# Optimization experiments

Measured on AMD Instinct MI355X. Metric: run time of the kernel, lower is better.

The kernel has to match this reference:

```python
import jax, jax.numpy as jnp
import numpy as np

B, S, HID, H = 4, 1024, 1024, 16
D = HID // H


def setup_inputs() -> dict:
    key = jax.random.key(0)
    ks = jax.random.split(key, 4)
    scale = 0.02
    return {
        "hidden_states": jax.random.normal(ks[0], (B, S, HID), dtype=jnp.float32),
        "attention_mask": jnp.ones((B, S), dtype=jnp.int32),
        "layer_head_mask": jnp.ones((H,), dtype=jnp.float32),
        "Wq": jax.random.normal(ks[1], (HID, HID), dtype=jnp.float32) * scale,
        "bq": jnp.zeros((HID,), dtype=jnp.float32),
        "Wk": jax.random.normal(ks[2], (HID, HID), dtype=jnp.float32) * scale,
        "bk": jnp.zeros((HID,), dtype=jnp.float32),
        "Wv": jax.random.normal(ks[3], (HID, HID), dtype=jnp.float32) * scale,
        "bv": jnp.zeros((HID,), dtype=jnp.float32),
    }


def reference(hidden_states, attention_mask, layer_head_mask, Wq, bq, Wk, bk, Wv, bv):
    b, s, _ = hidden_states.shape
    # QKV projections, split heads: [B,S,H,D]
    q = (hidden_states @ Wq + bq).reshape(b, s, H, D)
    k = (hidden_states @ Wk + bk).reshape(b, s, H, D)
    v = (hidden_states @ Wv + bv).reshape(b, s, H, D)

    # attention bias from padding mask: [B,1,1,S]
    mask = attention_mask[:, None, None, :]
    neg = jnp.finfo(jnp.float32).min
    bias = jnp.where(mask > 0, 0.0, neg).astype(jnp.float32)

    # dot_product_attention_weights: scale query by 1/sqrt(D)
    q = q / jnp.sqrt(jnp.asarray(D, dtype=q.dtype))
    scores = jnp.einsum("bqhd,bkhd->bhqk", q, k) + bias  # [B,H,S,S]
    attn_weights = jax.nn.softmax(scores, axis=-1)

    # per-head masking
    attn_weights = attn_weights * layer_head_mask[None, :, None, None]

    attn_output = jnp.einsum("bhqk,bkhd->bqhd", attn_weights, v)
    return attn_output.reshape(b, s, HID)
```

## Files before the change

kernel.cpp:

```cpp
#include <hip/hip_runtime.h>
#include <stdint.h>

typedef __bf16 bf16_t;
typedef bf16_t __attribute__((ext_vector_type(8))) bf16x8;
typedef float __attribute__((ext_vector_type(4))) f32x4;
typedef float __attribute__((ext_vector_type(16))) f32x16;
typedef unsigned u32;

#define BATCH 4
#define SEQ 1024
#define HIDD 1024
#define NH 16
#define DH 64

__device__ __forceinline__ unsigned short f2bf(float f) {
  unsigned u = __float_as_uint(f);
  u += 0x7fffu + ((u >> 16) & 1u);
  return (unsigned short)(u >> 16);
}

__device__ __forceinline__ f32x4 mfma16(bf16x8 a, bf16x8 b, f32x4 c) {
  return __builtin_amdgcn_mfma_f32_16x16x32_bf16(a, b, c, 0, 0, 0);
}
__device__ __forceinline__ f32x16 mfma32(bf16x8 a, bf16x8 b, f32x16 c) {
  return __builtin_amdgcn_mfma_f32_32x32x16_bf16(a, b, c, 0, 0, 0);
}

__device__ __forceinline__ void gload_lds16(const void* g, void* l) {
  __builtin_amdgcn_global_load_lds(
      (__attribute__((address_space(1))) void*)(uintptr_t)g,
      (__attribute__((address_space(3))) void*)l, 16, 0, 0);
}

__device__ __forceinline__ u32 cvtpk(float lo, float hi) {
  u32 r;
  asm("v_cvt_pk_bf16_f32 %0, %1, %2" : "=v"(r) : "v"(lo), "v"(hi));
  return r;
}
__device__ __forceinline__ void plswap(u32& a, u32& b) {
  asm("v_permlane32_swap_b32 %0, %1" : "+v"(a), "+v"(b));
}

__global__ __launch_bounds__(256) void prep(
    const float* __restrict__ hs, unsigned short* __restrict__ HSbf,
    const float* __restrict__ Wq, const float* __restrict__ Wk,
    const float* __restrict__ Wv, unsigned short* __restrict__ Wt) {
  __shared__ unsigned short tile[64][72];
  const int bid = blockIdx.x;
  if (bid < 4096) {
    const int i = bid * 256 + threadIdx.x;
    const float4 f = ((const float4*)hs)[i];
    ushort4 o = make_ushort4(f2bf(f.x), f2bf(f.y), f2bf(f.z), f2bf(f.w));
    ((ushort4*)HSbf)[i] = o;
    return;
  }
  const int id = bid - 4096;
  const int z = id >> 8, rem = id & 255;
  const int k0 = (rem & 15) * 64, n0 = (rem >> 4) * 64;
  const float* W = (z == 0) ? Wq : (z == 1) ? Wk : Wv;
  unsigned short* o = Wt + (size_t)z * (1024 * 1024);
  const int r = threadIdx.x >> 6, c = threadIdx.x & 63;
#pragma unroll
  for (int i = 0; i < 16; ++i) {
    const int row = i * 4 + r;
    tile[row][c] = f2bf(W[(size_t)(k0 + row) * 1024 + n0 + c]);
  }
  __syncthreads();
#pragma unroll
  for (int i = 0; i < 16; ++i) {
    const int row = i * 4 + r;
    o[(size_t)(n0 + row) * 1024 + k0 + c] = tile[c][row];
  }
}

__global__ __launch_bounds__(256) void qkv_gemm(
    const unsigned short* __restrict__ A,
    const unsigned short* __restrict__ Wt,
    const float* __restrict__ bq, const float* __restrict__ bk,
    const float* __restrict__ bv,
    unsigned short* __restrict__ Qb,
    unsigned short* __restrict__ Kpk,
    unsigned short* __restrict__ Vpk) {
  __shared__ alignas(16) unsigned short Alds[128 * 32];
  __shared__ alignas(16) unsigned short Blds[128 * 32];

  const int z = blockIdx.z;
  const unsigned short* Bt = Wt + (size_t)z * (1024 * 1024);
  const float* bias = (z == 0) ? bq : (z == 1) ? bk : bv;
  const float scale = (z == 0) ? 0.125f * 1.44269504089f : 1.0f;

  const int m0 = blockIdx.x * 128;
  const int n0 = blockIdx.y * 128;
  const int t = threadIdx.x;
  const int w = t >> 6, l = t & 63;
  const int lg = l >> 4, lc = l & 15;
  const int wr = w >> 1, wc = w & 1;

  f32x4 acc[4][4] = {};

  for (int kt = 0; kt < 1024; kt += 32) {
    __syncthreads();
#pragma unroll
    for (int i = 0; i < 2; ++i) {
      const int c = i * 256 + t;
      const int row = c >> 2;
      const int kp = (c & 3) * 8;
      gload_lds16(A + (size_t)(m0 + row) * 1024 + kt + kp,
                  (char*)Alds + i * 4096 + w * 1024);
      gload_lds16(Bt + (size_t)(n0 + row) * 1024 + kt + kp,
                  (char*)Blds + i * 4096 + w * 1024);
    }
    __syncthreads();

    bf16x8 af[4], bfr[4];
#pragma unroll
    for (int m = 0; m < 4; ++m)
      af[m] = *(const bf16x8*)(Alds + (wr * 64 + m * 16 + lc) * 32 + lg * 8);
#pragma unroll
    for (int n = 0; n < 4; ++n)
      bfr[n] = *(const bf16x8*)(Blds + (wc * 64 + n * 16 + lc) * 32 + lg * 8);
#pragma unroll
    for (int m = 0; m < 4; ++m)
#pragma unroll
      for (int n = 0; n < 4; ++n)
        acc[m][n] = mfma16(af[m], bfr[n], acc[m][n]);
  }

  if (z == 0) {
#pragma unroll
    for (int n = 0; n < 4; ++n) {
      const int col = n0 + wc * 64 + n * 16 + lc;
      const float bs = bias[col];
#pragma unroll
      for (int m = 0; m < 4; ++m)
#pragma unroll
        for (int r = 0; r < 4; ++r) {
          const int row = m0 + wr * 64 + m * 16 + lg * 4 + r;
          Qb[(size_t)row * 1024 + col] = f2bf((acc[m][n][r] + bs) * scale);
        }
    }
  } else if (z == 1) {
#pragma unroll
    for (int n = 0; n < 4; ++n) {
      const int col = n0 + wc * 64 + n * 16 + lc;
      const float bs = bias[col];
      const int h = col >> 6, s = (col >> 4) & 3, hi = (col >> 3) & 1, e = col & 7;
#pragma unroll
      for (int m = 0; m < 4; ++m)
#pragma unroll
        for (int r = 0; r < 4; ++r) {
          const int row = m0 + wr * 64 + m * 16 + lg * 4 + r;
          const int bh = (row >> 10) * 16 + h, tl = row & 1023;
          const int kb = tl >> 5, lo = tl & 31;
          Kpk[(size_t)(((bh * 32 + kb) * 4 + s) * 512) + (lo + hi * 32) * 8 + e] =
              f2bf(acc[m][n][r] + bs);
        }
    }
  } else {
#pragma unroll
    for (int n = 0; n < 4; ++n) {
      const int col = n0 + wc * 64 + n * 16 + lc;
      const float bs = bias[col];
      const int h = col >> 6, g = (col >> 5) & 1, lo = col & 31;
#pragma unroll
      for (int m = 0; m < 4; ++m)
#pragma unroll
        for (int r = 0; r < 4; ++r) {
          const int row = m0 + wr * 64 + m * 16 + lg * 4 + r;
          const int bh = (row >> 10) * 16 + h, tl = row & 1023;
          const int kt = tl >> 6, within = tl & 63;
          const int sv = within >> 4, hiv = (within >> 3) & 1, ev = within & 7;
          Vpk[(size_t)(((bh * 16 + kt) * 8 + g * 4 + sv) * 512) +
              (lo + hiv * 32) * 8 + ev] = f2bf(acc[m][n][r] + bs);
        }
    }
  }
}

__global__ __launch_bounds__(256, 2) void attn_kernel(
    const unsigned short* __restrict__ Qb,
    const unsigned short* __restrict__ Kpack,
    const unsigned short* __restrict__ Vpack,
    const int* __restrict__ amask,
    const float* __restrict__ lhm,
    float* __restrict__ out) {
  const int id = blockIdx.x;
  const int swzid = (id & 7) * 64 + (id >> 3);
  const int qt = swzid & 7;
  const int bh = swzid >> 3;
  const int b = bh >> 4, h = bh & 15;
  const int t = threadIdx.x;
  const int w = t >> 6, l = t & 63;
  const int lo = l & 31, hi = l >> 5;
  const int q0 = qt * 128 + w * 32;

  const unsigned short* Kp = Kpack + (size_t)bh * 65536 + l * 8;
  const unsigned short* Vp = Vpack + (size_t)bh * 65536 + l * 8;

  const unsigned short* qp = Qb + (size_t)(b * SEQ + q0 + lo) * HIDD + h * DH + hi * 8;
  bf16x8 qf[4];
#pragma unroll
  for (int s = 0; s < 4; ++s) qf[s] = *(const bf16x8*)(qp + s * 16);

  bool needmask;
  {
    unsigned long long mm = ~0ull;
#pragma unroll
    for (int tk = 0; tk < 16; ++tk)
      mm &= __ballot(amask[b * SEQ + tk * 64 + l] > 0);
    needmask = (mm != ~0ull);
  }

  float m_run = -INFINITY, l_run = 0.f;
  f32x16 acc0 = {}, acc1 = {};

  bf16x8 kf0[4], kf1[4], vf0[4], vf1[4];

#pragma unroll
  for (int s = 0; s < 4; ++s) {
    kf0[s] = *(const bf16x8*)(Kp + (s)*512);
    kf1[s] = *(const bf16x8*)(Kp + (4 + s) * 512);
  }

  for (int tk = 0; tk < 16; ++tk) {
#pragma unroll
    for (int s = 0; s < 4; ++s) {
      vf0[s] = *(const bf16x8*)(Vp + (size_t)(tk * 8 + s) * 512);
      vf1[s] = *(const bf16x8*)(Vp + (size_t)(tk * 8 + 4 + s) * 512);
    }

    f32x16 sg0 = {}, sg1 = {};
    __builtin_amdgcn_s_setprio(1);
#pragma unroll
    for (int s = 0; s < 4; ++s) {
      sg0 = mfma32(kf0[s], qf[s], sg0);
      sg1 = mfma32(kf1[s], qf[s], sg1);
    }
    __builtin_amdgcn_s_setprio(0);

    if (tk < 15) {
#pragma unroll
      for (int s = 0; s < 4; ++s) {
        kf0[s] = *(const bf16x8*)(Kp + (size_t)(tk * 8 + 8 + s) * 512);
        kf1[s] = *(const bf16x8*)(Kp + (size_t)(tk * 8 + 12 + s) * 512);
      }
    }

    float t0[8];
#pragma unroll
    for (int i = 0; i < 8; ++i)
      t0[i] = fmaxf(fmaxf(sg0[i], sg0[i + 8]), fmaxf(sg1[i], sg1[i + 8]));
    float t1 = fmaxf(fmaxf(fmaxf(t0[0], t0[1]), fmaxf(t0[2], t0[3])),
                     fmaxf(fmaxf(t0[4], t0[5]), fmaxf(t0[6], t0[7])));
    const float pmax = fmaxf(t1, __shfl_xor(t1, 32));

    if (!__all(pmax <= m_run + 8.f)) {
      const float mnew = fmaxf(m_run, pmax);
      const float sc = __builtin_amdgcn_exp2f(m_run - mnew);
      m_run = mnew;
      l_run *= sc;
#pragma unroll
      for (int g = 0; g < 16; ++g) {
        const int rowi = (g & 3) + 8 * (g >> 2) + 4 * hi;
        const float scr = __shfl(sc, rowi);
        acc0[g] *= scr;
        acc1[g] *= scr;
      }
    }

#pragma unroll
    for (int g = 0; g < 16; ++g) {
      sg0[g] = __builtin_amdgcn_exp2f(sg0[g] - m_run);
      sg1[g] = __builtin_amdgcn_exp2f(sg1[g] - m_run);
    }

    if (needmask) {
      const int mv = amask[b * SEQ + tk * 64 + l];
      const unsigned long long m64 = __ballot(mv > 0);
      if (m64 != ~0ull) {
#pragma unroll
        for (int g = 0; g < 16; ++g) {
          const int krow = (g & 3) + 8 * (g >> 2) + 4 * hi;
          if (!((m64 >> krow) & 1)) sg0[g] = 0.f;
          if (!((m64 >> (krow + 32)) & 1)) sg1[g] = 0.f;
        }
      }
    }

    float s0[8];
#pragma unroll
    for (int i = 0; i < 8; ++i)
      s0[i] = (sg0[i] + sg0[i + 8]) + (sg1[i] + sg1[i + 8]);
    float rs = ((s0[0] + s0[1]) + (s0[2] + s0[3])) +
               ((s0[4] + s0[5]) + (s0[6] + s0[7]));
    rs += __shfl_xor(rs, 32);
    l_run += rs;

    auto mk = [](float a0, float a1, float a2, float a3,
                 float a4, float a5, float a6, float a7) -> bf16x8 {
      u32 x = cvtpk(a0, a1), y = cvtpk(a2, a3);
      u32 a = cvtpk(a4, a5), b2 = cvtpk(a6, a7);
      plswap(x, a);
      plswap(y, b2);
      union { u32 u[4]; bf16x8 v; } fu;
      fu.u[0] = x; fu.u[1] = y; fu.u[2] = a; fu.u[3] = b2;
      return fu.v;
    };
    const bf16x8 pa0 = mk(sg0[0], sg0[1], sg0[2], sg0[3], sg0[4], sg0[5], sg0[6], sg0[7]);
    const bf16x8 pa1 = mk(sg0[8], sg0[9], sg0[10], sg0[11], sg0[12], sg0[13], sg0[14], sg0[15]);
    const bf16x8 pa2 = mk(sg1[0], sg1[1], sg1[2], sg1[3], sg1[4], sg1[5], sg1[6], sg1[7]);
    const bf16x8 pa3 = mk(sg1[8], sg1[9], sg1[10], sg1[11], sg1[12], sg1[13], sg1[14], sg1[15]);

    __builtin_amdgcn_s_setprio(1);
#pragma unroll
    for (int s = 0; s < 4; ++s) {
      const bf16x8 paf = (s == 0) ? pa0 : (s == 1) ? pa1 : (s == 2) ? pa2 : pa3;
      acc0 = mfma32(paf, vf0[s], acc0);
      acc1 = mfma32(paf, vf1[s], acc1);
    }
    __builtin_amdgcn_s_setprio(0);
  }

  const float hm = lhm[h];
  const float inv = hm / l_run;
  float* ob = out + (size_t)(b * SEQ + q0) * HIDD + h * DH + lo;
#pragma unroll
  for (int g = 0; g < 16; ++g) {
    const int rowi = (g & 3) + 8 * (g >> 2) + 4 * hi;
    const float iv = __shfl(inv, rowi);
    ob[(size_t)rowi * HIDD] = acc0[g] * iv;
    ob[(size_t)rowi * HIDD + 32] = acc1[g] * iv;
  }
}

extern "C" void kernel_launch(void* const* d_in, const int* in_sizes, int n_in,
                              void* d_out, int out_size, void* d_ws, size_t ws_size,
                              hipStream_t stream) {
  const float* hs = (const float*)d_in[0];
  const int* amask = (const int*)d_in[1];
  const float* lhm = (const float*)d_in[2];
  const float* Wq = (const float*)d_in[3];
  const float* bq = (const float*)d_in[4];
  const float* Wk = (const float*)d_in[5];
  const float* bk = (const float*)d_in[6];
  const float* Wv = (const float*)d_in[7];
  const float* bv = (const float*)d_in[8];
  float* out = (float*)d_out;

  char* ws = (char*)d_ws;
  unsigned short* HSbf = (unsigned short*)ws;
  unsigned short* Wt = (unsigned short*)(ws + (8u << 20));
  unsigned short* Qb = (unsigned short*)(ws + (14u << 20));
  unsigned short* Kpk = (unsigned short*)(ws + (22u << 20));
  unsigned short* Vpk = (unsigned short*)(ws + (30u << 20));

  prep<<<4864, 256, 0, stream>>>(hs, HSbf, Wq, Wk, Wv, Wt);
  qkv_gemm<<<dim3(32, 8, 3), 256, 0, stream>>>(HSbf, Wt, bq, bk, bv, Qb, Kpk, Vpk);
  attn_kernel<<<512, 256, 0, stream>>>(Qb, Kpk, Vpk, amask, lhm, out);
}
```

Measured before the change: 85.46 us.

## Pre-pack GEMM operands into MFMA fragment layout and load directly to registers

The prep kernel now writes the bf16 hidden states and transposed weights in a packed layout that matches the 16x16x32 MFMA fragment order. The QKV GEMM can then skip LDS and barriers entirely, loading fragments straight from global memory into registers with double-buffered prefetch. The grid is flattened and remapped so neighbouring blocks share A and B tiles, and launch bounds request three waves per SIMD. The cost is that each wave reads its own fragments from global memory, so there is no LDS reuse across waves and operand reuse depends on the L2 cache.

```diff
diff --git a/kernel.cpp b/kernel.cpp
--- a/kernel.cpp
+++ b/kernel.cpp
@@ -26,12 +26,6 @@
   return __builtin_amdgcn_mfma_f32_32x32x16_bf16(a, b, c, 0, 0, 0);
 }
 
-__device__ __forceinline__ void gload_lds16(const void* g, void* l) {
-  __builtin_amdgcn_global_load_lds(
-      (__attribute__((address_space(1))) void*)(uintptr_t)g,
-      (__attribute__((address_space(3))) void*)l, 16, 0, 0);
-}
-
 __device__ __forceinline__ u32 cvtpk(float lo, float hi) {
   u32 r;
   asm("v_cvt_pk_bf16_f32 %0, %1, %2" : "=v"(r) : "v"(lo), "v"(hi));
@@ -42,88 +36,105 @@
 }
 
 __global__ __launch_bounds__(256) void prep(
-    const float* __restrict__ hs, unsigned short* __restrict__ HSbf,
+    const float* __restrict__ hs, unsigned short* __restrict__ Apack,
     const float* __restrict__ Wq, const float* __restrict__ Wk,
-    const float* __restrict__ Wv, unsigned short* __restrict__ Wt) {
+    const float* __restrict__ Wv, unsigned short* __restrict__ Bpack) {
   __shared__ unsigned short tile[64][72];
   const int bid = blockIdx.x;
+  const int t = threadIdx.x;
   if (bid < 4096) {
-    const int i = bid * 256 + threadIdx.x;
-    const float4 f = ((const float4*)hs)[i];
+    const float4 f = ((const float4*)hs)[bid * 256 + t];
     ushort4 o = make_ushort4(f2bf(f.x), f2bf(f.y), f2bf(f.z), f2bf(f.w));
-    ((ushort4*)HSbf)[i] = o;
+    const int mt = bid >> 4, lc = bid & 15;
+    const int kt = t >> 3, lg = (t >> 1) & 3, e = (t & 1) * 4;
+    *(ushort4*)(Apack + (size_t)mt * 16384 + kt * 512 + (lg * 16 + lc) * 8 + e) = o;
     return;
   }
   const int id = bid - 4096;
   const int z = id >> 8, rem = id & 255;
   const int k0 = (rem & 15) * 64, n0 = (rem >> 4) * 64;
   const float* W = (z == 0) ? Wq : (z == 1) ? Wk : Wv;
-  unsigned short* o = Wt + (size_t)z * (1024 * 1024);
-  const int r = threadIdx.x >> 6, c = threadIdx.x & 63;
+  unsigned short* o = Bpack + (size_t)z * (1024 * 1024);
+  const int r = t >> 6, c = t & 63;
 #pragma unroll
   for (int i = 0; i < 16; ++i) {
     const int row = i * 4 + r;
     tile[row][c] = f2bf(W[(size_t)(k0 + row) * 1024 + n0 + c]);
   }
   __syncthreads();
-#pragma unroll
-  for (int i = 0; i < 16; ++i) {
-    const int row = i * 4 + r;
-    o[(size_t)(n0 + row) * 1024 + k0 + c] = tile[c][row];
-  }
-}
-
-__global__ __launch_bounds__(256) void qkv_gemm(
-    const unsigned short* __restrict__ A,
-    const unsigned short* __restrict__ Wt,
+  const int q = t >> 6, l = t & 63, lc = l & 15, lg = l >> 4;
+#pragma unroll
+  for (int it = 0; it < 2; ++it) {
+    const int nt = (rem >> 4) * 4 + q;
+    const int kt = (rem & 15) * 2 + it;
+    unsigned short buf[8];
+#pragma unroll
+    for (int e = 0; e < 8; ++e)
+      buf[e] = tile[it * 32 + lg * 8 + e][q * 16 + lc];
+    *(uint4*)(o + (size_t)nt * 16384 + kt * 512 + l * 8) = *(uint4*)buf;
+  }
+}
+
+__global__ __launch_bounds__(256, 3) void qkv_gemm(
+    const unsigned short* __restrict__ Apack,
+    const unsigned short* __restrict__ Bpack,
     const float* __restrict__ bq, const float* __restrict__ bk,
     const float* __restrict__ bv,
     unsigned short* __restrict__ Qb,
     unsigned short* __restrict__ Kpk,
     unsigned short* __restrict__ Vpk) {
-  __shared__ alignas(16) unsigned short Alds[128 * 32];
-  __shared__ alignas(16) unsigned short Blds[128 * 32];
-
-  const int z = blockIdx.z;
-  const unsigned short* Bt = Wt + (size_t)z * (1024 * 1024);
+  const int id = blockIdx.x;
+  const int j = id >> 3;
+  const int mx = (id & 7) * 4 + (j & 3);
+  const int rest = j >> 2;
+  const int nx = rest & 7;
+  const int z = rest >> 3;
+
   const float* bias = (z == 0) ? bq : (z == 1) ? bk : bv;
   const float scale = (z == 0) ? 0.125f * 1.44269504089f : 1.0f;
-
-  const int m0 = blockIdx.x * 128;
-  const int n0 = blockIdx.y * 128;
+  const int m0 = mx * 128, n0 = nx * 128;
   const int t = threadIdx.x;
   const int w = t >> 6, l = t & 63;
   const int lg = l >> 4, lc = l & 15;
   const int wr = w >> 1, wc = w & 1;
 
+  const unsigned short* Ap = Apack + (size_t)(mx * 8 + wr * 4) * 16384 + l * 8;
+  const unsigned short* Bp = Bpack + (size_t)z * (1024 * 1024) +
+                             (size_t)(nx * 8 + wc * 4) * 16384 + l * 8;
+
   f32x4 acc[4][4] = {};
-
-  for (int kt = 0; kt < 1024; kt += 32) {
-    __syncthreads();
-#pragma unroll
-    for (int i = 0; i < 2; ++i) {
-      const int c = i * 256 + t;
-      const int row = c >> 2;
-      const int kp = (c & 3) * 8;
-      gload_lds16(A + (size_t)(m0 + row) * 1024 + kt + kp,
-                  (char*)Alds + i * 4096 + w * 1024);
-      gload_lds16(Bt + (size_t)(n0 + row) * 1024 + kt + kp,
-                  (char*)Blds + i * 4096 + w * 1024);
-    }
-    __syncthreads();
-
-    bf16x8 af[4], bfr[4];
+  bf16x8 a0[4], b0[4], a1[4], b1[4];
+
+#pragma unroll
+  for (int m = 0; m < 4; ++m) {
+    a0[m] = *(const bf16x8*)(Ap + m * 16384);
+    b0[m] = *(const bf16x8*)(Bp + m * 16384);
+  }
+
+  for (int kk = 0; kk < 16; ++kk) {
+    const int kt = kk * 2;
+#pragma unroll
+    for (int m = 0; m < 4; ++m) {
+      a1[m] = *(const bf16x8*)(Ap + m * 16384 + (kt + 1) * 512);
+      b1[m] = *(const bf16x8*)(Bp + m * 16384 + (kt + 1) * 512);
+    }
 #pragma unroll
     for (int m = 0; m < 4; ++m)
-      af[m] = *(const bf16x8*)(Alds + (wr * 64 + m * 16 + lc) * 32 + lg * 8);
-#pragma unroll
-    for (int n = 0; n < 4; ++n)
-      bfr[n] = *(const bf16x8*)(Blds + (wc * 64 + n * 16 + lc) * 32 + lg * 8);
+#pragma unroll
+      for (int n = 0; n < 4; ++n)
+        acc[m][n] = mfma16(a0[m], b0[n], acc[m][n]);
+    if (kk < 15) {
+#pragma unroll
+      for (int m = 0; m < 4; ++m) {
+        a0[m] = *(const bf16x8*)(Ap + m * 16384 + (kt + 2) * 512);
+        b0[m] = *(const bf16x8*)(Bp + m * 16384 + (kt + 2) * 512);
+      }
+    }
 #pragma unroll
     for (int m = 0; m < 4; ++m)
 #pragma unroll
       for (int n = 0; n < 4; ++n)
-        acc[m][n] = mfma16(af[m], bfr[n], acc[m][n]);
+        acc[m][n] = mfma16(a1[m], b1[n], acc[m][n]);
   }
 
   if (z == 0) {
@@ -348,13 +359,13 @@
   float* out = (float*)d_out;
 
   char* ws = (char*)d_ws;
-  unsigned short* HSbf = (unsigned short*)ws;
-  unsigned short* Wt = (unsigned short*)(ws + (8u << 20));
+  unsigned short* Apack = (unsigned short*)ws;
+  unsigned short* Bpack = (unsigned short*)(ws + (8u << 20));
   unsigned short* Qb = (unsigned short*)(ws + (14u << 20));
   unsigned short* Kpk = (unsigned short*)(ws + (22u << 20));
   unsigned short* Vpk = (unsigned short*)(ws + (30u << 20));
 
-  prep<<<4864, 256, 0, stream>>>(hs, HSbf, Wq, Wk, Wv, Wt);
-  qkv_gemm<<<dim3(32, 8, 3), 256, 0, stream>>>(HSbf, Wt, bq, bk, bv, Qb, Kpk, Vpk);
+  prep<<<4864, 256, 0, stream>>>(hs, Apack, Wq, Wk, Wv, Bpack);
+  qkv_gemm<<<768, 256, 0, stream>>>(Apack, Bpack, bq, bk, bv, Qb, Kpk, Vpk);
   attn_kernel<<<512, 256, 0, stream>>>(Qb, Kpk, Vpk, amask, lhm, out);
 }
```

After: 79.32 us. 1.08x faster.
